# Kernel tuning notes

Measured on AMD Instinct MI355X. Metric: run time of the kernel, lower is better.

Reference implementation:

```python
import jax, jax.numpy as jnp
import numpy as np

N = 8192        # num nodes
E = 262144      # edges per relation (avg degree 32)
R = 2           # number of edge relations in edge_index_dict
F = 111         # num_feature
D = 32          # embedding_dim
H = 256         # hidden_dim
C = 15          # num_classes (pooled cluster count)


def setup_inputs() -> dict:
    key = jax.random.key(0)
    ks = jax.random.split(key, 9)
    x_note = jax.random.normal(ks[0], (N, F), dtype=jnp.float32)
    edges = jax.random.randint(ks[1], (R, 2, E), 0, N, dtype=jnp.int32)
    s = 0.1
    W_embed = jax.random.normal(ks[2], (F, D), dtype=jnp.float32) * s
    b_embed = jnp.zeros((D,), jnp.float32)
    W_self = jax.random.normal(ks[3], (R, D, H), dtype=jnp.float32) * s
    W_neigh = jax.random.normal(ks[4], (R, D, H), dtype=jnp.float32) * s
    b_gnn = jnp.zeros((R, H), jnp.float32)
    W_s1 = jax.random.normal(ks[5], (H, C), dtype=jnp.float32) * s
    W_s2 = jax.random.normal(ks[6], (H, C), dtype=jnp.float32) * s
    return dict(x_note=x_note, edges=edges, W_embed=W_embed, b_embed=b_embed,
                W_self=W_self, W_neigh=W_neigh, b_gnn=b_gnn, W_s1=W_s1, W_s2=W_s2)


def _coord_to_adj(edges, n):
    # edges: [R, 2, E] -> dense adjacency [R, n, n] via a single scatter per relation
    def one(e):
        return jnp.zeros((n, n), jnp.float32).at[e[0], e[1]].set(1.0)
    return jax.vmap(one)(edges)


def _hetero_gnn(x, edges, W_self, W_neigh, b, n):
    # per-relation SAGEConv (mean aggregation), summed over relations, ReLU
    def one(e, ws, wn, bb):
        src, dst = e[0], e[1]
        msg_sum = jax.ops.segment_sum(x[src], dst, num_segments=n)      # [n, D]
        cnt = jax.ops.segment_sum(jnp.ones((e.shape[1],), x.dtype), dst, num_segments=n)
        mean = msg_sum / jnp.maximum(cnt, 1.0)[:, None]
        return x @ ws + mean @ wn + bb
    outs = jax.vmap(one)(edges, W_self, W_neigh, b)  # [R, n, H]
    return jax.nn.relu(outs.sum(0))


def _gnn_cluster(x, adj, W_s):
    # DiffPool-style: S = softmax(A_sum X W_s); X' = S^T X; A'_r = S^T A_r S
    a_sum = adj.sum(0)                                  # [n, n]
    S = jax.nn.softmax((a_sum @ x) @ W_s, axis=-1)      # [n, C]
    x_p = S.T @ x                                       # [C, H]
    tmp = jnp.einsum('rnm,mc->rnc', adj, S)             # [R, n, C]
    adj_p = jnp.einsum('nk,rnc->rkc', S, tmp)           # [R, C, C]
    return x_p, adj_p, S


def reference(x_note, edges, W_embed, b_embed, W_self, W_neigh, b_gnn, W_s1, W_s2):
    n = x_note.shape[0]
    x = x_note @ W_embed + b_embed                      # linear_embed
    adj = _coord_to_adj(edges, n)                       # coord_to_adj
    x = _hetero_gnn(x, edges, W_self, W_neigh, b_gnn, n)  # gnn_embed
    x, adj, S1 = _gnn_cluster(x, adj, W_s1)             # gnn_cluster1
    x, adj, S2 = _gnn_cluster(x, adj, W_s2)             # gnn_cluster2
    return (x, S1, S2)
```

## Files before the change

kernel.cpp:

```cpp
#include <hip/hip_runtime.h>
#include <hip/hip_bf16.h>

#define N_NODES 8192
#define E_EDGES 262144
#define R_REL   2
#define F_FEAT  111
#define D_EMB   32
#define H_HID   256
#define C_CLS   15
#define DCAP2   96
#define SCAP    96


__global__ void k_prep(const float* __restrict__ x_note, const float* __restrict__ W,
                       const float* __restrict__ b, float* __restrict__ X0,
                       const int* __restrict__ edges, int* __restrict__ deg,
                       int* __restrict__ colD2,
                       const float* __restrict__ Wself, const float* __restrict__ Wneigh,
                       float* __restrict__ W96) {
    int blk = blockIdx.x;
    if (blk < 1024) {
        __shared__ float Ws[F_FEAT * D_EMB];
        for (int i = threadIdx.x; i < F_FEAT * D_EMB; i += blockDim.x) Ws[i] = W[i];
        __syncthreads();
        int tid = blk * 256 + threadIdx.x;
        int n = tid >> 5, d = tid & 31;
        const float* xr = x_note + n * F_FEAT;
        float acc = b[d];
        for (int f = 0; f < F_FEAT; ++f) acc += xr[f] * Ws[f * D_EMB + d];
        X0[n * D_EMB + d] = acc;
    } else if (blk < 3072) {
        int i = (blk - 1024) * 256 + threadIdx.x;
        int r = i >> 18, e = i & (E_EDGES - 1);
        int src = edges[(r * 2) * E_EDGES + e];
        int dst = edges[(r * 2 + 1) * E_EDGES + e];
        int pos = atomicAdd(&deg[(2 + r) * N_NODES + dst], 1);
        if (pos < DCAP2) colD2[(r * N_NODES + dst) * DCAP2 + pos] = src;
    } else {
        int i = (blk - 3072) * 256 + threadIdx.x;
        int dd = i >> 8, h = i & 255;
        float v;
        if (dd < 32)      v = Wself[dd * 256 + h] + Wself[(32 + dd) * 256 + h];
        else if (dd < 64) v = Wneigh[(dd - 32) * 256 + h];
        else              v = Wneigh[(32 + dd - 64) * 256 + h];
        W96[i] = v;
    }
}

__global__ __launch_bounds__(256) void k_dedup_mean(const int* __restrict__ degIn,
                                                    const int* __restrict__ colD2,
                                                    int* __restrict__ deg,
                                                    int* __restrict__ colS2,
                                                    const float* __restrict__ X0,
                                                    float* __restrict__ xin) {
    int blk = blockIdx.x;
    if (blk < 4096) {
        __shared__ int buf[4][DCAP2];
        int w = threadIdx.x >> 6, lane = threadIdx.x & 63;
        int row = blk * 4 + w;
        int r = row >> 13, n = row & (N_NODES - 1);
        int lenRaw = degIn[(2 + r) * N_NODES + n];
        int lim = (lenRaw < DCAP2) ? lenRaw : DCAP2;
        const int* base = colD2 + (r * N_NODES + n) * DCAP2;
        for (int i = lane; i < lim; i += 64) buf[w][i] = base[i];
        __syncthreads();
        int v0 = (lane < lim) ? buf[w][lane] : -1;
        int v1 = (lane + 64 < lim) ? buf[w][lane + 64] : -1;
        bool d0 = false, d1 = false;
        for (int j = 0; j < lim; ++j) {
            int vj = buf[w][j];
            if (j < lane && vj == v0) d0 = true;
            if (j < lane + 64 && vj == v1) d1 = true;
        }
        if (lane < lim && !d0) {
            int pos = atomicAdd(&deg[r * N_NODES + v0], 1);
            if (pos < SCAP) colS2[(r * N_NODES + v0) * SCAP + pos] = n;
        }
        if (lane + 64 < lim && !d1) {
            int pos = atomicAdd(&deg[r * N_NODES + v1], 1);
            if (pos < SCAP) colS2[(r * N_NODES + v1) * SCAP + pos] = n;
        }
    } else {
        int p = (blk - 4096) * 8 + (threadIdx.x >> 5);
        int d = threadIdx.x & 31;
        int n = p >> 1, r = p & 1;
        int lenRaw = degIn[(2 + r) * N_NODES + n];
        int len = (lenRaw < DCAP2) ? lenRaw : DCAP2;
        const int* cr = colD2 + (r * N_NODES + n) * DCAP2;
        float a0 = 0.f, a1 = 0.f, a2 = 0.f, a3 = 0.f;
        int idx = 0;
        for (; idx + 4 <= len; idx += 4) {
            int c0 = cr[idx], c1 = cr[idx + 1], c2 = cr[idx + 2], c3 = cr[idx + 3];
            a0 += X0[c0 * D_EMB + d]; a1 += X0[c1 * D_EMB + d];
            a2 += X0[c2 * D_EMB + d]; a3 += X0[c3 * D_EMB + d];
        }
        for (; idx < len; ++idx) a0 += X0[cr[idx] * D_EMB + d];
        float inv = 1.f / fmaxf((float)lenRaw, 1.f);
        xin[n * 96 + 32 + r * 32 + d] = ((a0 + a1) + (a2 + a3)) * inv;
        if (r == 0) xin[n * 96 + d] = X0[n * D_EMB + d];
    }
}

__global__ __launch_bounds__(256) void k_gemm_g1(const float* __restrict__ xin,
                                                 const float* __restrict__ W96,
                                                 const float* __restrict__ bg,
                                                 const float* __restrict__ Ws1,
                                                 float* __restrict__ H1,
                                                 float* __restrict__ G1) {
    __shared__ float As[64][97];
    __shared__ float Bs[96][64];
    int g = blockIdx.x;
    int bm = g >> 2, bn = g & 3;
    int t = threadIdx.x;
    int nb = bm * 64, cb = bn * 64;
    for (int i = t; i < 64 * 96; i += 256) { int row = i / 96, k = i - row * 96; As[row][k] = xin[(nb + row) * 96 + k]; }
    for (int i = t; i < 96 * 64; i += 256) { int k = i >> 6, col = i & 63; Bs[k][col] = W96[k * 256 + cb + col]; }
    __syncthreads();
    int tx = t & 15, ty = t >> 4;
    float acc[4][4] = {};
    #pragma unroll 4
    for (int k = 0; k < 96; ++k) {
        float a0 = As[ty * 4 + 0][k], a1 = As[ty * 4 + 1][k], a2 = As[ty * 4 + 2][k], a3 = As[ty * 4 + 3][k];
        float b0 = Bs[k][tx * 4 + 0], b1 = Bs[k][tx * 4 + 1], b2 = Bs[k][tx * 4 + 2], b3 = Bs[k][tx * 4 + 3];
        acc[0][0] += a0 * b0; acc[0][1] += a0 * b1; acc[0][2] += a0 * b2; acc[0][3] += a0 * b3;
        acc[1][0] += a1 * b0; acc[1][1] += a1 * b1; acc[1][2] += a1 * b2; acc[1][3] += a1 * b3;
        acc[2][0] += a2 * b0; acc[2][1] += a2 * b1; acc[2][2] += a2 * b2; acc[2][3] += a2 * b3;
        acc[3][0] += a3 * b0; acc[3][1] += a3 * b1; acc[3][2] += a3 * b2; acc[3][3] += a3 * b3;
    }
    float hv[4][4];
    #pragma unroll
    for (int i = 0; i < 4; ++i) {
        int n = nb + ty * 4 + i;
        #pragma unroll
        for (int j = 0; j < 4; ++j) {
            int c = cb + tx * 4 + j;
            hv[i][j] = fmaxf(acc[i][j] + bg[c] + bg[H_HID + c], 0.f);
            H1[n * H_HID + c] = hv[i][j];
        }
    }
    __syncthreads();
    float* Wg = &Bs[0][0];
    #pragma unroll
    for (int i = 0; i < 4; ++i)
        #pragma unroll
        for (int j = 0; j < 4; ++j)
            As[ty * 4 + i][tx * 4 + j] = hv[i][j];
    for (int idx = t; idx < 64 * C_CLS; idx += 256) {
        int j = idx / C_CLS, c = idx - j * C_CLS;
        Wg[j * 16 + c] = Ws1[(cb + j) * C_CLS + c];
    }
    __syncthreads();
    for (int task = t; task < 64 * C_CLS; task += 256) {
        int row = task / C_CLS, c = task - row * C_CLS;
        float s = 0.f;
        #pragma unroll 8
        for (int j = 0; j < 64; ++j) s += As[row][j] * Wg[j * 16 + c];
        atomicAdd(&G1[(nb + row) * 16 + c], s);
    }
}

__global__ __launch_bounds__(256) void k_logits_sm(const int* __restrict__ deg,
                                                   const int* __restrict__ colS2,
                                                   const float* __restrict__ G1,
                                                   float* __restrict__ S1,
                                                   float* __restrict__ S1p) {
    int n = (blockIdx.x * blockDim.x + threadIdx.x) >> 4;
    int c = threadIdx.x & 15;
    float a0 = 0.f, a1 = 0.f, a2 = 0.f, a3 = 0.f, a4 = 0.f, a5 = 0.f, a6 = 0.f, a7 = 0.f;
    for (int r = 0; r < R_REL; ++r) {
        int len = deg[r * N_NODES + n];
        if (len > SCAP) len = SCAP;
        const int* cr = colS2 + (r * N_NODES + n) * SCAP;
        int idx = 0;
        for (; idx + 8 <= len; idx += 8) {
            int c0 = cr[idx + 0], c1 = cr[idx + 1], c2 = cr[idx + 2], c3 = cr[idx + 3];
            int c4 = cr[idx + 4], c5 = cr[idx + 5], c6 = cr[idx + 6], c7 = cr[idx + 7];
            a0 += G1[c0 * 16 + c]; a1 += G1[c1 * 16 + c];
            a2 += G1[c2 * 16 + c]; a3 += G1[c3 * 16 + c];
            a4 += G1[c4 * 16 + c]; a5 += G1[c5 * 16 + c];
            a6 += G1[c6 * 16 + c]; a7 += G1[c7 * 16 + c];
        }
        for (; idx < len; ++idx) a0 += G1[cr[idx] * 16 + c];
    }
    float logit = (c < C_CLS) ? (((a0 + a1) + (a2 + a3)) + ((a4 + a5) + (a6 + a7))) : -1e30f;
    float m = logit;
    for (int off = 8; off; off >>= 1) m = fmaxf(m, __shfl_xor(m, off, 16));
    float e = (c < C_CLS) ? expf(logit - m) : 0.f;
    float ssum = e;
    for (int off = 8; off; off >>= 1) ssum += __shfl_xor(ssum, off, 16);
    float p = e / ssum;
    if (c < C_CLS) S1[n * C_CLS + c] = p;
    S1p[n * 16 + c] = (c < C_CLS) ? p : 0.f;
}

__global__ __launch_bounds__(256) void k_xpT(const float* __restrict__ S1p, const float* __restrict__ H1,
                                             float* __restrict__ xp,
                                             const int* __restrict__ deg, const int* __restrict__ colS2,
                                             float* __restrict__ partial) {
    __shared__ float Tl[16][16];
    int blk = blockIdx.x;
    if (blk < 128) {
        int h = threadIdx.x;
        int base = blk * 64;
        float acc[C_CLS];
        #pragma unroll
        for (int c = 0; c < C_CLS; ++c) acc[c] = 0.f;
        for (int i = 0; i < 64; ++i) {
            int n = base + i;
            float hv = H1[n * H_HID + h];
            const float* sr = S1p + n * 16;
            #pragma unroll
            for (int c = 0; c < C_CLS; ++c) acc[c] += sr[c] * hv;
        }
        #pragma unroll
        for (int c = 0; c < C_CLS; ++c) atomicAdd(&xp[c * H_HID + h], acc[c]);
    } else {
        int bb = blk - 128;
        int g = threadIdx.x >> 4, c = threadIdx.x & 15;
        int n0 = bb * 16;
        int n = n0 + g;
        float a0 = 0.f, a1 = 0.f, a2 = 0.f, a3 = 0.f, a4 = 0.f, a5 = 0.f, a6 = 0.f, a7 = 0.f;
        for (int r = 0; r < R_REL; ++r) {
            int len = deg[r * N_NODES + n];
            if (len > SCAP) len = SCAP;
            const int* cr = colS2 + (r * N_NODES + n) * SCAP;
            int idx = 0;
            for (; idx + 8 <= len; idx += 8) {
                int c0 = cr[idx + 0], c1 = cr[idx + 1], c2 = cr[idx + 2], c3 = cr[idx + 3];
                int c4 = cr[idx + 4], c5 = cr[idx + 5], c6 = cr[idx + 6], c7 = cr[idx + 7];
                a0 += S1p[c0 * 16 + c]; a1 += S1p[c1 * 16 + c];
                a2 += S1p[c2 * 16 + c]; a3 += S1p[c3 * 16 + c];
                a4 += S1p[c4 * 16 + c]; a5 += S1p[c5 * 16 + c];
                a6 += S1p[c6 * 16 + c]; a7 += S1p[c7 * 16 + c];
            }
            for (; idx < len; ++idx) a0 += S1p[cr[idx] * 16 + c];
        }
        float tval = ((a0 + a1) + (a2 + a3)) + ((a4 + a5) + (a6 + a7));
        Tl[g][c] = (c < C_CLS) ? tval : 0.f;
        __syncthreads();
        int t = threadIdx.x;
        if (t < C_CLS * C_CLS) {
            int k = t / C_CLS, cc = t - k * C_CLS;
            float s = 0.f;
            #pragma unroll
            for (int i = 0; i < 16; ++i) s += S1p[(n0 + i) * 16 + k] * Tl[i][cc];
            partial[bb * (C_CLS * C_CLS) + t] = s;
        }
    }
}

__global__ void k_cluster2(const float* __restrict__ partialAdj, const float* __restrict__ xp,
                           const float* __restrict__ Ws2, float* __restrict__ out_x,
                           float* __restrict__ out_S2) {
    __shared__ float a2[C_CLS * C_CLS];
    __shared__ float xps[C_CLS * H_HID];
    __shared__ float y2[C_CLS * H_HID];
    __shared__ float lg[C_CLS * C_CLS];
    __shared__ float S2s[C_CLS * C_CLS];
    int t = threadIdx.x;
    if (t < C_CLS * C_CLS) {
        float s0 = 0.f, s1 = 0.f, s2 = 0.f, s3 = 0.f;
        for (int b = 0; b < 512; b += 4) {
            s0 += partialAdj[(b + 0) * (C_CLS * C_CLS) + t];
            s1 += partialAdj[(b + 1) * (C_CLS * C_CLS) + t];
            s2 += partialAdj[(b + 2) * (C_CLS * C_CLS) + t];
            s3 += partialAdj[(b + 3) * (C_CLS * C_CLS) + t];
        }
        a2[t] = (s0 + s1) + (s2 + s3);
    }
    for (int i = t; i < C_CLS * H_HID; i += 256) xps[i] = xp[i];
    __syncthreads();
    for (int i = 0; i < C_CLS; ++i) {
        float acc = 0.f;
        #pragma unroll
        for (int j = 0; j < C_CLS; ++j) acc += a2[i * C_CLS + j] * xps[j * H_HID + t];
        y2[i * H_HID + t] = acc;
    }
    __syncthreads();
    for (int idx = t; idx < C_CLS * C_CLS; idx += 256) {
        int i = idx / C_CLS, c = idx % C_CLS;
        float acc = 0.f;
        for (int h = 0; h < H_HID; ++h) acc += y2[i * H_HID + h] * Ws2[h * C_CLS + c];
        lg[idx] = acc;
    }
    __syncthreads();
    if (t < C_CLS) {
        float m = -1e30f;
        for (int c = 0; c < C_CLS; ++c) m = fmaxf(m, lg[t * C_CLS + c]);
        float s = 0.f;
        for (int c = 0; c < C_CLS; ++c) { float ev = expf(lg[t * C_CLS + c] - m); S2s[t * C_CLS + c] = ev; s += ev; }
        for (int c = 0; c < C_CLS; ++c) { S2s[t * C_CLS + c] /= s; out_S2[t * C_CLS + c] = S2s[t * C_CLS + c]; }
    }
    __syncthreads();
    for (int c = 0; c < C_CLS; ++c) {
        float acc = 0.f;
        #pragma unroll
        for (int i = 0; i < C_CLS; ++i) acc += S2s[i * C_CLS + c] * xps[i * H_HID + t];
        out_x[c * H_HID + t] = acc;
    }
}

extern "C" void kernel_launch(void* const* d_in, const int* in_sizes, int n_in,
                              void* d_out, int out_size, void* d_ws, size_t ws_size,
                              hipStream_t stream) {
    const float* x_note  = (const float*)d_in[0];
    const int*   edges   = (const int*)d_in[1];
    const float* W_embed = (const float*)d_in[2];
    const float* b_embed = (const float*)d_in[3];
    const float* W_self  = (const float*)d_in[4];
    const float* W_neigh = (const float*)d_in[5];
    const float* b_gnn   = (const float*)d_in[6];
    const float* W_s1    = (const float*)d_in[7];
    const float* W_s2    = (const float*)d_in[8];
    float* out = (float*)d_out;

    float* out_x  = out;
    float* out_S1 = out + C_CLS * H_HID;
    float* out_S2 = out + C_CLS * H_HID + N_NODES * C_CLS;

    char* ws = (char*)d_ws;
    size_t off = 0;
    auto alloc = [&](size_t bytes) { size_t p = off; off += (bytes + 255) & ~(size_t)255; return p; };
    size_t regionA = alloc((size_t)18 * 1024 * 1024);
    size_t oDeg    = alloc((size_t)4 * N_NODES * 4);
    size_t oXp     = alloc((size_t)C_CLS * H_HID * 4);
    size_t oG1     = alloc((size_t)N_NODES * 16 * 4);
    size_t zeroEnd = off;
    size_t oX0     = alloc((size_t)N_NODES * D_EMB * 4);
    size_t oPart   = alloc((size_t)512 * C_CLS * C_CLS * 4);
    size_t oW96    = alloc((size_t)96 * H_HID * 4);

    int*   colD2  = (int*)(ws + regionA);
    float* H1     = (float*)(ws + regionA);
    int*   colS2  = (int*)(ws + regionA + (size_t)8 * 1024 * 1024);
    float* S1p    = (float*)(ws + regionA + (size_t)14 * 1024 * 1024);
    float* xin    = (float*)(ws + regionA + (size_t)14 * 1024 * 1024 + 512 * 1024);
    int*   deg    = (int*)(ws + oDeg);
    float* xp     = (float*)(ws + oXp);
    float* G1     = (float*)(ws + oG1);
    float* X0     = (float*)(ws + oX0);
    float* partialAdj = (float*)(ws + oPart);
    float* W96    = (float*)(ws + oW96);

    hipMemsetAsync(ws + oDeg, 0, zeroEnd - oDeg, stream);

    k_prep<<<3168, 256, 0, stream>>>(x_note, W_embed, b_embed, X0, edges, deg, colD2,
                                     W_self, W_neigh, W96);
    k_dedup_mean<<<4096 + 2048, 256, 0, stream>>>(deg, colD2, deg, colS2, X0, xin);
    k_gemm_g1<<<512, 256, 0, stream>>>(xin, W96, b_gnn, W_s1, H1, G1);
    k_logits_sm<<<(N_NODES * 16) / 256, 256, 0, stream>>>(deg, colS2, G1, out_S1, S1p);
    k_xpT<<<128 + 512, 256, 0, stream>>>(S1p, H1, xp, deg, colS2, partialAdj);
    k_cluster2<<<1, 256, 0, stream>>>(partialAdj, xp, W_s2, out_x, out_S2);
}
```

Baseline: 142.8 us.

## Fuse neighbor-mean gather into dedup kernel and dedup with LDS bitmap

Each wavefront now does two jobs for one (relation, node) row. It deduplicates the row's source list with an atomicOr into a per-wave 8192-bit LDS bitmap, replacing the quadratic pairwise comparison loop. It then reuses the neighbor indices already staged in LDS to compute the mean aggregation, splitting the list across two half-waves that are combined with a shuffle. This removes the separate 2048 mean-aggregation blocks and their second read of colD2. In exchange, each wave must zero a 1 KB bitmap and issue LDS atomics.

```diff
diff --git a/kernel.cpp b/kernel.cpp
--- a/kernel.cpp
+++ b/kernel.cpp
@@ -10,6 +10,7 @@
 #define C_CLS   15
 #define DCAP2   96
 #define SCAP    96
+#define BMW     256
 
 
 __global__ void k_prep(const float* __restrict__ x_note, const float* __restrict__ W,
@@ -47,56 +48,47 @@
     }
 }
 
-__global__ __launch_bounds__(256) void k_dedup_mean(const int* __restrict__ degIn,
+__global__ __launch_bounds__(256) void k_dedup_mean(const int* __restrict__ deg,
                                                     const int* __restrict__ colD2,
-                                                    int* __restrict__ deg,
+                                                    int* __restrict__ degS,
                                                     int* __restrict__ colS2,
                                                     const float* __restrict__ X0,
                                                     float* __restrict__ xin) {
-    int blk = blockIdx.x;
-    if (blk < 4096) {
-        __shared__ int buf[4][DCAP2];
-        int w = threadIdx.x >> 6, lane = threadIdx.x & 63;
-        int row = blk * 4 + w;
-        int r = row >> 13, n = row & (N_NODES - 1);
-        int lenRaw = degIn[(2 + r) * N_NODES + n];
-        int lim = (lenRaw < DCAP2) ? lenRaw : DCAP2;
-        const int* base = colD2 + (r * N_NODES + n) * DCAP2;
-        for (int i = lane; i < lim; i += 64) buf[w][i] = base[i];
-        __syncthreads();
-        int v0 = (lane < lim) ? buf[w][lane] : -1;
-        int v1 = (lane + 64 < lim) ? buf[w][lane + 64] : -1;
-        bool d0 = false, d1 = false;
-        for (int j = 0; j < lim; ++j) {
-            int vj = buf[w][j];
-            if (j < lane && vj == v0) d0 = true;
-            if (j < lane + 64 && vj == v1) d1 = true;
-        }
-        if (lane < lim && !d0) {
-            int pos = atomicAdd(&deg[r * N_NODES + v0], 1);
-            if (pos < SCAP) colS2[(r * N_NODES + v0) * SCAP + pos] = n;
-        }
-        if (lane + 64 < lim && !d1) {
-            int pos = atomicAdd(&deg[r * N_NODES + v1], 1);
-            if (pos < SCAP) colS2[(r * N_NODES + v1) * SCAP + pos] = n;
-        }
-    } else {
-        int p = (blk - 4096) * 8 + (threadIdx.x >> 5);
-        int d = threadIdx.x & 31;
-        int n = p >> 1, r = p & 1;
-        int lenRaw = degIn[(2 + r) * N_NODES + n];
-        int len = (lenRaw < DCAP2) ? lenRaw : DCAP2;
-        const int* cr = colD2 + (r * N_NODES + n) * DCAP2;
-        float a0 = 0.f, a1 = 0.f, a2 = 0.f, a3 = 0.f;
-        int idx = 0;
-        for (; idx + 4 <= len; idx += 4) {
-            int c0 = cr[idx], c1 = cr[idx + 1], c2 = cr[idx + 2], c3 = cr[idx + 3];
-            a0 += X0[c0 * D_EMB + d]; a1 += X0[c1 * D_EMB + d];
-            a2 += X0[c2 * D_EMB + d]; a3 += X0[c3 * D_EMB + d];
-        }
-        for (; idx < len; ++idx) a0 += X0[cr[idx] * D_EMB + d];
+    __shared__ int buf[4][DCAP2];
+    __shared__ unsigned int bm[4][BMW];
+    int w = threadIdx.x >> 6, lane = threadIdx.x & 63;
+    int row = blockIdx.x * 4 + w;
+    int r = row >> 13, n = row & (N_NODES - 1);
+    int lenRaw = deg[(2 + r) * N_NODES + n];
+    int lim = (lenRaw < DCAP2) ? lenRaw : DCAP2;
+    const int* base = colD2 + (r * N_NODES + n) * DCAP2;
+    #pragma unroll
+    for (int q = 0; q < BMW / 64; ++q) bm[w][lane + q * 64] = 0u;
+    for (int i = lane; i < lim; i += 64) buf[w][i] = base[i];
+    __syncthreads();
+    for (int i = lane; i < lim; i += 64) {
+        int v = buf[w][i];
+        unsigned int bit = 1u << (v & 31);
+        unsigned int old = atomicOr(&bm[w][v >> 5], bit);
+        if (!(old & bit)) {
+            int pos = atomicAdd(&degS[r * N_NODES + v], 1);
+            if (pos < SCAP) colS2[(r * N_NODES + v) * SCAP + pos] = n;
+        }
+    }
+    int d = lane & 31, h = lane >> 5;
+    float a0 = 0.f, a1 = 0.f, a2 = 0.f, a3 = 0.f;
+    int i = h;
+    for (; i + 6 < lim; i += 8) {
+        int c0 = buf[w][i], c1 = buf[w][i + 2], c2 = buf[w][i + 4], c3 = buf[w][i + 6];
+        a0 += X0[c0 * D_EMB + d]; a1 += X0[c1 * D_EMB + d];
+        a2 += X0[c2 * D_EMB + d]; a3 += X0[c3 * D_EMB + d];
+    }
+    for (; i < lim; i += 2) a0 += X0[buf[w][i] * D_EMB + d];
+    float acc = ((a0 + a1) + (a2 + a3));
+    acc += __shfl_down(acc, 32, 64);
+    if (lane < 32) {
         float inv = 1.f / fmaxf((float)lenRaw, 1.f);
-        xin[n * 96 + 32 + r * 32 + d] = ((a0 + a1) + (a2 + a3)) * inv;
+        xin[n * 96 + 32 + r * 32 + d] = acc * inv;
         if (r == 0) xin[n * 96 + d] = X0[n * D_EMB + d];
     }
 }
@@ -346,7 +338,7 @@
 
     k_prep<<<3168, 256, 0, stream>>>(x_note, W_embed, b_embed, X0, edges, deg, colD2,
                                      W_self, W_neigh, W96);
-    k_dedup_mean<<<4096 + 2048, 256, 0, stream>>>(deg, colD2, deg, colS2, X0, xin);
+    k_dedup_mean<<<4096, 256, 0, stream>>>(deg, colD2, deg, colS2, X0, xin);
     k_gemm_g1<<<512, 256, 0, stream>>>(xin, W96, b_gnn, W_s1, H1, G1);
     k_logits_sm<<<(N_NODES * 16) / 256, 256, 0, stream>>>(deg, colS2, G1, out_S1, S1p);
     k_xpT<<<128 + 512, 256, 0, stream>>>(S1p, H1, xp, deg, colS2, partialAdj);
```

Result: faster. 135.5 us (-5.1%).
